# Optimization experiments

Measured on AMD Instinct MI355X. Metric: run time of the kernel, lower is better.

## Reference

```python
import jax, jax.numpy as jnp
import numpy as np

B, C, Q, E = 32, 1024, 64, 256  # batch, max_context_len, max_question_len, embedding_size
FE = 4 * E                      # final_encoding_size (self_attention=False)


def setup_inputs() -> dict:
    key = jax.random.key(0)
    ks = jax.random.split(key, 7)
    return {
        "context": jax.random.normal(ks[0], (B, C, E), dtype=jnp.float32),
        "question": jax.random.normal(ks[1], (B, Q, E), dtype=jnp.float32),
        "context_mask": jnp.ones((B, C), dtype=jnp.float32),
        "w_question": jax.random.normal(ks[2], (E,), dtype=jnp.float32),
        "w_context": jax.random.normal(ks[3], (E,), dtype=jnp.float32),
        "w_multiple": jax.random.normal(ks[4], (E,), dtype=jnp.float32),
        "final_W": jax.random.normal(ks[5], (FE, FE), dtype=jnp.float32) * (1.0 / np.sqrt(FE)),
        "final_b": jnp.zeros((FE,), dtype=jnp.float32),
    }


def reference(context, question, context_mask, w_question, w_context, w_multiple, final_W, final_b):
    # Trilinear similarity: s[b,c,q] = <w_q, q_q> + <w_c, c_c> + <w_m, c_c * q_q>
    q_weighted = question @ w_question                 # (B, Q)
    ctx_weighted = context @ w_context                 # (B, C)
    # (question.unsqueeze(1) * context.unsqueeze(2)) @ w_multiple, computed
    # without materializing the (B, C, Q, E) intermediate:
    mult = jnp.einsum('bce,bqe->bcq', context * w_multiple, question)  # (B, C, Q)
    similarity = ctx_weighted[:, :, None] + q_weighted[:, None, :] + mult  # (B, C, Q)

    # Context-to-query attention (softmax over question dim)
    c2q_att = jnp.einsum('bcq,bqe->bce', jax.nn.softmax(similarity, axis=2), question)

    # Query-to-context attention (softmax over context dim of row-max scores)
    q2c_weights = jax.nn.softmax(jnp.max(similarity, axis=2), axis=1)   # (B, C)
    q2c_att = jnp.einsum('bc,bce->be', q2c_weights, context)            # (B, E)

    attended = jnp.concatenate(
        [context, c2q_att, context * c2q_att, context * q2c_att[:, None, :]],
        axis=2)                                                          # (B, C, 4E)

    # MaskedLinear: affine map, output rows zeroed where context_mask == 0
    out = (attended @ final_W.T + final_b) * context_mask[:, :, None]    # (B, C, 4E)
    return out
```

## Files before the change

kernel.cpp:

```cpp
#include <hip/hip_runtime.h>

#define BB 32
#define CC 1024
#define QQ 64
#define EE 256
#define FE 1024
#define MM (BB*CC)

typedef __bf16 bf16_t;
typedef bf16_t bf16x8 __attribute__((ext_vector_type(8)));
typedef float f32x4 __attribute__((ext_vector_type(4)));

__device__ __forceinline__ unsigned short f2bf(float f) {
  unsigned u = __float_as_uint(f);
  u += 0x7fffu + ((u >> 16) & 1u);
  return (unsigned short)(u >> 16);
}
__device__ __forceinline__ float bf2f(unsigned short u) {
  return __uint_as_float(((unsigned)u) << 16);
}

__device__ __forceinline__ void gload_lds16(const void* g, void* l) {
  __builtin_amdgcn_global_load_lds(
      (const __attribute__((address_space(1))) unsigned int*)g,
      (__attribute__((address_space(3))) unsigned int*)l, 16, 0, 0);
}

__global__ void k_prep_q(const float* __restrict__ question, const float* __restrict__ w_question,
                         const float* __restrict__ w_multiple, float* __restrict__ qm,
                         float* __restrict__ qw) {
  int gid = blockIdx.x * 256 + threadIdx.x;
  int row = gid >> 6;
  int lane = gid & 63;
  const float4 q = *(const float4*)(question + (size_t)row * EE + lane * 4);
  const float4 wm = *(const float4*)(w_multiple + lane * 4);
  const float4 wq = *(const float4*)(w_question + lane * 4);
  float4 r; r.x = q.x*wm.x; r.y = q.y*wm.y; r.z = q.z*wm.z; r.w = q.w*wm.w;
  *(float4*)(qm + (size_t)row * EE + lane * 4) = r;
  float d = q.x*wq.x + q.y*wq.y + q.z*wq.z + q.w*wq.w;
  d += __shfl_xor(d, 1);  d += __shfl_xor(d, 2);  d += __shfl_xor(d, 4);
  d += __shfl_xor(d, 8);  d += __shfl_xor(d, 16); d += __shfl_xor(d, 32);
  if (lane == 0) qw[row] = d;
}

__global__ void k_cast_w(const float* __restrict__ W, unsigned short* __restrict__ Wb) {
  int i = (blockIdx.x * 256 + threadIdx.x) * 4;
  float4 v = *(const float4*)(W + i);
  ushort4 o; o.x = f2bf(v.x); o.y = f2bf(v.y); o.z = f2bf(v.z); o.w = f2bf(v.w);
  *(ushort4*)(Wb + i) = o;
}

#define DOT4(acc, A, Bv) acc += A.x*Bv.x + A.y*Bv.y + A.z*Bv.z + A.w*Bv.w

__launch_bounds__(256)
__global__ void k_sim(const float* __restrict__ ctx, const float* __restrict__ qm,
                      const float* __restrict__ qw_g, const float* __restrict__ w_context,
                      float* __restrict__ P, float* __restrict__ rowmax,
                      unsigned short* __restrict__ att) {
  __shared__ float qml[QQ][260];
  __shared__ float ck[64][36];
  __shared__ float cwl[64];
  __shared__ float qwl[QQ];
  const int tid = threadIdx.x;
  const int b = blockIdx.y;
  const int c0 = blockIdx.x * 64;
  const int tx = tid & 15, ty = tid >> 4;

  const float* qmb = qm + (size_t)b * (QQ * EE);
  for (int idx = tid * 4; idx < QQ * EE; idx += 1024) {
    float4 v = *(const float4*)(qmb + idx);
    *(float4*)&qml[idx >> 8][idx & 255] = v;
  }
  if (tid < QQ) qwl[tid] = qw_g[b * QQ + tid];

  const int cr = tid >> 3, er = (tid & 7) * 4;
  const float* crow0 = ctx + ((size_t)(b * CC + c0 + cr)) * EE;
  const float* crow1 = crow0 + 32 * EE;
  unsigned short* arow0 = att + ((size_t)(b * CC + c0 + cr)) * FE;
  unsigned short* arow1 = arow0 + (size_t)32 * FE;
  float s[4][4] = {{0.f}};
  float cp0 = 0.f, cp1 = 0.f;

  for (int eo = 0; eo < EE; eo += 32) {
    float4 cv0 = *(const float4*)(crow0 + eo + er);
    float4 cv1 = *(const float4*)(crow1 + eo + er);
    float4 wc = *(const float4*)(w_context + eo + er);
    cp0 += cv0.x*wc.x + cv0.y*wc.y + cv0.z*wc.z + cv0.w*wc.w;
    cp1 += cv1.x*wc.x + cv1.y*wc.y + cv1.z*wc.z + cv1.w*wc.w;
    ushort4 u0, u1;
    u0.x = f2bf(cv0.x); u0.y = f2bf(cv0.y); u0.z = f2bf(cv0.z); u0.w = f2bf(cv0.w);
    u1.x = f2bf(cv1.x); u1.y = f2bf(cv1.y); u1.z = f2bf(cv1.z); u1.w = f2bf(cv1.w);
    *(ushort4*)(arow0 + eo + er) = u0;
    *(ushort4*)(arow1 + eo + er) = u1;
    __syncthreads();
    *(float4*)&ck[cr][er] = cv0;
    *(float4*)&ck[cr + 32][er] = cv1;
    __syncthreads();
#pragma unroll
    for (int ee = 0; ee < 32; ee += 4) {
      float4 a0 = *(const float4*)&ck[ty +  0][ee];
      float4 a1 = *(const float4*)&ck[ty + 16][ee];
      float4 a2 = *(const float4*)&ck[ty + 32][ee];
      float4 a3 = *(const float4*)&ck[ty + 48][ee];
      float4 b0 = *(const float4*)&qml[tx +  0][eo + ee];
      float4 b1 = *(const float4*)&qml[tx + 16][eo + ee];
      float4 b2 = *(const float4*)&qml[tx + 32][eo + ee];
      float4 b3 = *(const float4*)&qml[tx + 48][eo + ee];
      DOT4(s[0][0], a0, b0); DOT4(s[0][1], a0, b1); DOT4(s[0][2], a0, b2); DOT4(s[0][3], a0, b3);
      DOT4(s[1][0], a1, b0); DOT4(s[1][1], a1, b1); DOT4(s[1][2], a1, b2); DOT4(s[1][3], a1, b3);
      DOT4(s[2][0], a2, b0); DOT4(s[2][1], a2, b1); DOT4(s[2][2], a2, b2); DOT4(s[2][3], a2, b3);
      DOT4(s[3][0], a3, b0); DOT4(s[3][1], a3, b1); DOT4(s[3][2], a3, b2); DOT4(s[3][3], a3, b3);
    }
  }
  cp0 += __shfl_xor(cp0, 1); cp0 += __shfl_xor(cp0, 2); cp0 += __shfl_xor(cp0, 4);
  cp1 += __shfl_xor(cp1, 1); cp1 += __shfl_xor(cp1, 2); cp1 += __shfl_xor(cp1, 4);
  if ((tid & 7) == 0) { cwl[cr] = cp0; cwl[cr + 32] = cp1; }
  __syncthreads();

#pragma unroll
  for (int i = 0; i < 4; ++i) {
    int c = ty + 16 * i;
    float cw = cwl[c];
    float f[4], mx = -1e30f;
#pragma unroll
    for (int j = 0; j < 4; ++j) {
      f[j] = s[i][j] + cw + qwl[tx + 16 * j];
      mx = fmaxf(mx, f[j]);
    }
    mx = fmaxf(mx, __shfl_xor(mx, 1));
    mx = fmaxf(mx, __shfl_xor(mx, 2));
    mx = fmaxf(mx, __shfl_xor(mx, 4));
    mx = fmaxf(mx, __shfl_xor(mx, 8));
    float sum = 0.f;
#pragma unroll
    for (int j = 0; j < 4; ++j) { f[j] = expf(f[j] - mx); sum += f[j]; }
    sum += __shfl_xor(sum, 1);
    sum += __shfl_xor(sum, 2);
    sum += __shfl_xor(sum, 4);
    sum += __shfl_xor(sum, 8);
    float inv = 1.f / sum;
    if (tx == 0) rowmax[(size_t)b * CC + c0 + c] = mx;
    size_t prow = ((size_t)(b * CC + c0 + c)) * QQ;
#pragma unroll
    for (int j = 0; j < 4; ++j) P[prow + tx + 16 * j] = f[j] * inv;
  }
}

__global__ void k_q2c_softmax(const float* __restrict__ rowmax, float* __restrict__ q2cw) {
  int b = blockIdx.x, tid = threadIdx.x;
  __shared__ float rbuf[4], sbuf[4];
  float4 v = *(const float4*)(rowmax + (size_t)b * CC + tid * 4);
  float m = fmaxf(fmaxf(v.x, v.y), fmaxf(v.z, v.w));
  for (int off = 1; off < 64; off <<= 1) m = fmaxf(m, __shfl_xor(m, off));
  int wv = tid >> 6;
  if ((tid & 63) == 0) rbuf[wv] = m;
  __syncthreads();
  m = fmaxf(fmaxf(rbuf[0], rbuf[1]), fmaxf(rbuf[2], rbuf[3]));
  float e0 = expf(v.x - m), e1 = expf(v.y - m), e2 = expf(v.z - m), e3 = expf(v.w - m);
  float sum = e0 + e1 + e2 + e3;
  for (int off = 1; off < 64; off <<= 1) sum += __shfl_xor(sum, off);
  if ((tid & 63) == 0) sbuf[wv] = sum;
  __syncthreads();
  sum = sbuf[0] + sbuf[1] + sbuf[2] + sbuf[3];
  float inv = 1.f / sum;
  float4 o; o.x = e0 * inv; o.y = e1 * inv; o.z = e2 * inv; o.w = e3 * inv;
  *(float4*)(q2cw + (size_t)b * CC + tid * 4) = o;
}

__global__ void k_q2c_part(const unsigned short* __restrict__ att, const float* __restrict__ w,
                           float* __restrict__ part) {
  int b = blockIdx.y, ch = blockIdx.x;
  int e = threadIdx.x;
  const unsigned short* base = att + ((size_t)(b * CC + ch * 128)) * FE + e;
  const float* wp = w + b * CC + ch * 128;
  float acc = 0.f;
#pragma unroll 4
  for (int c = 0; c < 128; ++c) acc += wp[c] * bf2f(base[(size_t)c * FE]);
  part[(b * 8 + ch) * EE + e] = acc;
}

__global__ void k_q2c_sum(const float* __restrict__ part, float* __restrict__ q2catt) {
  int b = blockIdx.x, e = threadIdx.x;
  float a = 0.f;
#pragma unroll
  for (int ch = 0; ch < 8; ++ch) a += part[(b * 8 + ch) * EE + e];
  q2catt[b * EE + e] = a;
}

__launch_bounds__(256)
__global__ void k_pv(const float* __restrict__ P, const float* __restrict__ question,
                     const float* __restrict__ q2catt, unsigned short* __restrict__ attended) {
  __shared__ float PT[QQ][65];
  __shared__ float ql[QQ][68];
  const int tid = threadIdx.x;
  const int b = blockIdx.y, c0 = blockIdx.x * 64;
  const int tx = tid & 15, ty = tid >> 4;

  {
    int q4 = (tid & 15) * 4, cb = tid >> 4;
#pragma unroll
    for (int r = 0; r < 4; ++r) {
      int c = cb + 16 * r;
      float4 v = *(const float4*)(P + ((size_t)(b * CC + c0 + c)) * QQ + q4);
      PT[q4 + 0][c] = v.x; PT[q4 + 1][c] = v.y; PT[q4 + 2][c] = v.z; PT[q4 + 3][c] = v.w;
    }
  }
  const float* qb = question + (size_t)b * (QQ * EE);
  const float* g2 = q2catt + b * EE;

  for (int ep = 0; ep < EE; ep += 64) {
    __syncthreads();
    {
      int q = tid >> 2, e16 = (tid & 3) * 16;
      const float* src = qb + (size_t)q * EE + ep + e16;
      float4 v0 = *(const float4*)(src);
      float4 v1 = *(const float4*)(src + 4);
      float4 v2 = *(const float4*)(src + 8);
      float4 v3 = *(const float4*)(src + 12);
      *(float4*)&ql[q][e16]      = v0;
      *(float4*)&ql[q][e16 + 4]  = v1;
      *(float4*)&ql[q][e16 + 8]  = v2;
      *(float4*)&ql[q][e16 + 12] = v3;
    }
    __syncthreads();
    float s[4][4] = {{0.f}};
#pragma unroll 8
    for (int q = 0; q < QQ; ++q) {
      float a0 = PT[q][ty];
      float a1 = PT[q][ty + 16];
      float a2 = PT[q][ty + 32];
      float a3 = PT[q][ty + 48];
      float4 bv = *(const float4*)&ql[q][tx * 4];
      s[0][0] += a0 * bv.x; s[0][1] += a0 * bv.y; s[0][2] += a0 * bv.z; s[0][3] += a0 * bv.w;
      s[1][0] += a1 * bv.x; s[1][1] += a1 * bv.y; s[1][2] += a1 * bv.z; s[1][3] += a1 * bv.w;
      s[2][0] += a2 * bv.x; s[2][1] += a2 * bv.y; s[2][2] += a2 * bv.z; s[2][3] += a2 * bv.w;
      s[3][0] += a3 * bv.x; s[3][1] += a3 * bv.y; s[3][2] += a3 * bv.z; s[3][3] += a3 * bv.w;
    }
    float4 gv = *(const float4*)(g2 + ep + tx * 4);
#pragma unroll
    for (int i = 0; i < 4; ++i) {
      int c = ty + 16 * i;
      size_t row = (size_t)(b * CC + c0 + c);
      unsigned short* arow = attended + row * (size_t)FE;
      ushort4 cu = *(const ushort4*)(arow + 0 * EE + ep + tx * 4);
      float cx = bf2f(cu.x), cy = bf2f(cu.y), cz = bf2f(cu.z), cw = bf2f(cu.w);
      ushort4 s1, s2, s3;
      s1.x = f2bf(s[i][0]);        s1.y = f2bf(s[i][1]);        s1.z = f2bf(s[i][2]);        s1.w = f2bf(s[i][3]);
      s2.x = f2bf(cx * s[i][0]);   s2.y = f2bf(cy * s[i][1]);   s2.z = f2bf(cz * s[i][2]);   s2.w = f2bf(cw * s[i][3]);
      s3.x = f2bf(cx * gv.x);      s3.y = f2bf(cy * gv.y);      s3.z = f2bf(cz * gv.z);      s3.w = f2bf(cw * gv.w);
      *(ushort4*)(arow + 1 * EE + ep + tx * 4) = s1;
      *(ushort4*)(arow + 2 * EE + ep + tx * 4) = s2;
      *(ushort4*)(arow + 3 * EE + ep + tx * 4) = s3;
    }
  }
}

__launch_bounds__(512, 2)
__global__ void k_gemm(const unsigned short* __restrict__ A, const unsigned short* __restrict__ Bw,
                       const float* __restrict__ bias, const float* __restrict__ mask,
                       float* __restrict__ out) {
  __shared__ bf16_t As[2][256][64];
  __shared__ bf16_t Bs[2][256][64];
  const int tid = threadIdx.x;
  const int lane = tid & 63;
  const int wave = tid >> 6;
  const int wr = wave >> 2;
  const int wc = wave & 3;

  const int bid = blockIdx.x;
  const int wg = (bid & 7) * 64 + (bid >> 3);
  const int brow = (wg >> 2) * 256;
  const int bcol = (wg & 3) * 256;

  const int r = lane & 15, kg4 = lane >> 4;
  const int lxor = lane & 7;

  const int srow = tid >> 3;
  const int sg = (tid & 7) ^ (srow & 7);
  const unsigned short* gA = A  + (size_t)(brow + srow) * FE + sg * 8;
  const unsigned short* gB = Bw + (size_t)(bcol + srow) * FE + sg * 8;
  bf16_t* ldsA = &As[0][srow][(tid & 7) * 8];
  bf16_t* ldsB = &Bs[0][srow][(tid & 7) * 8];

  f32x4 acc[8][4] = {};

#define STAGE(bufi, t)                                                          \
  {                                                                             \
    const int k0 = (t) * 64;                                                    \
    _Pragma("unroll")                                                           \
    for (int r0 = 0; r0 < 256; r0 += 64) {                                      \
      gload_lds16(gA + (size_t)r0 * FE + k0, ldsA + (size_t)(bufi) * (256*64) + r0 * 64); \
      gload_lds16(gB + (size_t)r0 * FE + k0, ldsB + (size_t)(bufi) * (256*64) + r0 * 64); \
    }                                                                           \
  }

  STAGE(0, 0);
  STAGE(1, 1);

  for (int t = 0; t < 16; ++t) {
    const int cur = t & 1;
    if (t < 15) {
      asm volatile("s_waitcnt vmcnt(8)" ::: "memory");
    } else {
      asm volatile("s_waitcnt vmcnt(0)" ::: "memory");
    }
    __builtin_amdgcn_s_barrier();

    bf16x8 fa[8][2], fb[4][2];
#pragma unroll
    for (int m = 0; m < 8; ++m) {
      const int rowa = wr * 128 + m * 16 + r;
#pragma unroll
      for (int ks = 0; ks < 2; ++ks)
        fa[m][ks] = *(const bf16x8*)&As[cur][rowa][((ks * 4 + kg4) ^ lxor) * 8];
    }
#pragma unroll
    for (int n = 0; n < 4; ++n) {
      const int rowb = wc * 64 + n * 16 + r;
#pragma unroll
      for (int ks = 0; ks < 2; ++ks)
        fb[n][ks] = *(const bf16x8*)&Bs[cur][rowb][((ks * 4 + kg4) ^ lxor) * 8];
    }
    asm volatile("s_waitcnt lgkmcnt(0)" ::: "memory");
    __builtin_amdgcn_s_barrier();

    if (t < 14) STAGE(cur, t + 2);

    __builtin_amdgcn_s_setprio(1);
#pragma unroll
    for (int ks = 0; ks < 2; ++ks)
#pragma unroll
      for (int m = 0; m < 8; ++m)
#pragma unroll
        for (int n = 0; n < 4; ++n)
          acc[m][n] = __builtin_amdgcn_mfma_f32_16x16x32_bf16(fa[m][ks], fb[n][ks], acc[m][n], 0, 0, 0);
    __builtin_amdgcn_s_setprio(0);
  }
#undef STAGE

#pragma unroll
  for (int m = 0; m < 8; ++m) {
#pragma unroll
    for (int n = 0; n < 4; ++n) {
#pragma unroll
      for (int reg = 0; reg < 4; ++reg) {
        int row = brow + wr * 128 + m * 16 + kg4 * 4 + reg;
        int col = bcol + wc * 64 + n * 16 + r;
        out[(size_t)row * FE + col] = (acc[m][n][reg] + bias[col]) * mask[row];
      }
    }
  }
}

extern "C" void kernel_launch(void* const* d_in, const int* in_sizes, int n_in,
                              void* d_out, int out_size, void* d_ws, size_t ws_size,
                              hipStream_t stream) {
  const float* ctx  = (const float*)d_in[0];
  const float* ques = (const float*)d_in[1];
  const float* mask = (const float*)d_in[2];
  const float* w_q  = (const float*)d_in[3];
  const float* w_c  = (const float*)d_in[4];
  const float* w_m  = (const float*)d_in[5];
  const float* fW   = (const float*)d_in[6];
  const float* fb   = (const float*)d_in[7];
  float* out = (float*)d_out;

  char* ws = (char*)d_ws;
  float* qm     = (float*)(ws);
  float* qw     = (float*)(ws + 8388608);
  float* rowmax = (float*)(ws + 8396800);
  float* q2cw   = (float*)(ws + 8527872);
  float* part   = (float*)(ws + 8658944);
  float* q2catt = (float*)(ws + 8921088);
  float* P      = (float*)(ws + 8953856);
  unsigned short* attended = (unsigned short*)(ws + 17342464);
  unsigned short* Wb       = (unsigned short*)(ws + 84451328);

  k_prep_q<<<512, 256, 0, stream>>>(ques, w_q, w_m, qm, qw);
  k_cast_w<<<1024, 256, 0, stream>>>(fW, Wb);
  k_sim<<<dim3(16, 32), 256, 0, stream>>>(ctx, qm, qw, w_c, P, rowmax, attended);
  k_q2c_softmax<<<32, 256, 0, stream>>>(rowmax, q2cw);
  k_q2c_part<<<dim3(8, 32), 256, 0, stream>>>(attended, q2cw, part);
  k_q2c_sum<<<32, 256, 0, stream>>>(part, q2catt);
  k_pv<<<dim3(16, 32), 256, 0, stream>>>(P, ques, q2catt, attended);
  k_gemm<<<512, 512, 0, stream>>>(attended, Wb, fb, mask, out);
}
```

Baseline: 178.5 us.

## Restructure GEMM main loop into 8-wave ping-pong with split half-tile staging

Rewrites the bf16 GEMM main loop so each K-tile's A and B are staged as two 128-row halves. LDS fragment reads, global-to-LDS loads and four MFMA sub-blocks are interleaved per iteration under frequent barriers and partial vmcnt waits. The aim is to overlap global loads and LDS reads with MFMA work at finer grain than whole-tile double buffering. It adds many barriers and a tightly choreographed wait scheme that may serialize waves or carry subtle race risks.

```diff
diff --git a/kernel.cpp b/kernel.cpp
--- a/kernel.cpp
+++ b/kernel.cpp
@@ -259,13 +259,14 @@
 __global__ void k_gemm(const unsigned short* __restrict__ A, const unsigned short* __restrict__ Bw,
                        const float* __restrict__ bias, const float* __restrict__ mask,
                        float* __restrict__ out) {
-  __shared__ bf16_t As[2][256][64];
-  __shared__ bf16_t Bs[2][256][64];
+  __shared__ bf16_t As[2][2][128][64];
+  __shared__ bf16_t Bs[2][2][128][64];
   const int tid = threadIdx.x;
   const int lane = tid & 63;
   const int wave = tid >> 6;
   const int wr = wave >> 2;
   const int wc = wave & 3;
+  const int bh = wc >> 1;
 
   const int bid = blockIdx.x;
   const int wg = (bid & 7) * 64 + (bid >> 3);
@@ -273,70 +274,100 @@
   const int bcol = (wg & 3) * 256;
 
   const int r = lane & 15, kg4 = lane >> 4;
-  const int lxor = lane & 7;
+  const int rx = r & 7;
 
   const int srow = tid >> 3;
   const int sg = (tid & 7) ^ (srow & 7);
-  const unsigned short* gA = A  + (size_t)(brow + srow) * FE + sg * 8;
-  const unsigned short* gB = Bw + (size_t)(bcol + srow) * FE + sg * 8;
-  bf16_t* ldsA = &As[0][srow][(tid & 7) * 8];
-  bf16_t* ldsB = &Bs[0][srow][(tid & 7) * 8];
+  const unsigned short* gAb = A  + (size_t)(brow + srow) * FE + sg * 8;
+  const unsigned short* gBb = Bw + (size_t)(bcol + srow) * FE + sg * 8;
+  bf16_t* ldsAb = &As[0][0][srow][(tid & 7) * 8];
+  bf16_t* ldsBb = &Bs[0][0][srow][(tid & 7) * 8];
 
   f32x4 acc[8][4] = {};
-
-#define STAGE(bufi, t)                                                          \
-  {                                                                             \
-    const int k0 = (t) * 64;                                                    \
-    _Pragma("unroll")                                                           \
-    for (int r0 = 0; r0 < 256; r0 += 64) {                                      \
-      gload_lds16(gA + (size_t)r0 * FE + k0, ldsA + (size_t)(bufi) * (256*64) + r0 * 64); \
-      gload_lds16(gB + (size_t)r0 * FE + k0, ldsB + (size_t)(bufi) * (256*64) + r0 * 64); \
-    }                                                                           \
-  }
-
-  STAGE(0, 0);
-  STAGE(1, 1);
-
-  for (int t = 0; t < 16; ++t) {
-    const int cur = t & 1;
-    if (t < 15) {
-      asm volatile("s_waitcnt vmcnt(8)" ::: "memory");
-    } else {
-      asm volatile("s_waitcnt vmcnt(0)" ::: "memory");
-    }
-    __builtin_amdgcn_s_barrier();
-
-    bf16x8 fa[8][2], fb[4][2];
-#pragma unroll
-    for (int m = 0; m < 8; ++m) {
-      const int rowa = wr * 128 + m * 16 + r;
-#pragma unroll
-      for (int ks = 0; ks < 2; ++ks)
-        fa[m][ks] = *(const bf16x8*)&As[cur][rowa][((ks * 4 + kg4) ^ lxor) * 8];
-    }
-#pragma unroll
-    for (int n = 0; n < 4; ++n) {
-      const int rowb = wc * 64 + n * 16 + r;
-#pragma unroll
-      for (int ks = 0; ks < 2; ++ks)
-        fb[n][ks] = *(const bf16x8*)&Bs[cur][rowb][((ks * 4 + kg4) ^ lxor) * 8];
-    }
-    asm volatile("s_waitcnt lgkmcnt(0)" ::: "memory");
-    __builtin_amdgcn_s_barrier();
-
-    if (t < 14) STAGE(cur, t + 2);
-
-    __builtin_amdgcn_s_setprio(1);
-#pragma unroll
-    for (int ks = 0; ks < 2; ++ks)
-#pragma unroll
-      for (int m = 0; m < 8; ++m)
-#pragma unroll
-        for (int n = 0; n < 4; ++n)
-          acc[m][n] = __builtin_amdgcn_mfma_f32_16x16x32_bf16(fa[m][ks], fb[n][ks], acc[m][n], 0, 0, 0);
-    __builtin_amdgcn_s_setprio(0);
-  }
-#undef STAGE
+  bf16x8 faA[4][2], faB[4][2], fbA[2][2], fbB[2][2];
+
+#define BARX __builtin_amdgcn_s_barrier()
+#define LGKM0 do { asm volatile("s_waitcnt lgkmcnt(0)" ::: "memory"); __builtin_amdgcn_sched_barrier(0); } while (0)
+#define VMW4 asm volatile("s_waitcnt vmcnt(4)" ::: "memory")
+#define VMW0 asm volatile("s_waitcnt vmcnt(0)" ::: "memory")
+
+#define ST_A(SLOT, H, KOFF) do {                                              \
+    const unsigned short* s_ = gAb + (size_t)((H) * 128) * FE + (KOFF);       \
+    bf16_t* d_ = ldsAb + ((SLOT) * 2 + (H)) * (128 * 64);                     \
+    gload_lds16(s_, d_);                                                      \
+    gload_lds16(s_ + (size_t)64 * FE, d_ + 64 * 64);                          \
+  } while (0)
+#define ST_B(SLOT, H, KOFF) do {                                              \
+    const unsigned short* s_ = gBb + (size_t)((H) * 128) * FE + (KOFF);       \
+    bf16_t* d_ = ldsBb + ((SLOT) * 2 + (H)) * (128 * 64);                     \
+    gload_lds16(s_, d_);                                                      \
+    gload_lds16(s_ + (size_t)64 * FE, d_ + 64 * 64);                          \
+  } while (0)
+
+#define RD_FA(DST, SLOT, MB) do {                                             \
+    _Pragma("unroll") for (int mm = 0; mm < 4; ++mm) {                        \
+      const int row_ = ((MB) + mm) * 16 + r;                                  \
+      _Pragma("unroll") for (int ks = 0; ks < 2; ++ks)                        \
+        DST[mm][ks] = *(const bf16x8*)&As[SLOT][wr][row_][((ks * 4 + kg4) ^ rx) * 8]; \
+    } } while (0)
+#define RD_FB(DST, SLOT, NB) do {                                             \
+    _Pragma("unroll") for (int nn = 0; nn < 2; ++nn) {                        \
+      const int row_ = (wc & 1) * 64 + ((NB) + nn) * 16 + r;                  \
+      _Pragma("unroll") for (int ks = 0; ks < 2; ++ks)                        \
+        DST[nn][ks] = *(const bf16x8*)&Bs[SLOT][bh][row_][((ks * 4 + kg4) ^ rx) * 8]; \
+    } } while (0)
+
+#define MFMA16(FA, FB, MB, NB) do {                                           \
+    __builtin_amdgcn_s_setprio(1);                                            \
+    _Pragma("unroll") for (int ks = 0; ks < 2; ++ks)                          \
+    _Pragma("unroll") for (int mm = 0; mm < 4; ++mm)                          \
+    _Pragma("unroll") for (int nn = 0; nn < 2; ++nn)                          \
+      acc[(MB) + mm][(NB) + nn] = __builtin_amdgcn_mfma_f32_16x16x32_bf16(    \
+          FA[mm][ks], FB[nn][ks], acc[(MB) + mm][(NB) + nn], 0, 0, 0);        \
+    __builtin_amdgcn_s_setprio(0);                                            \
+  } while (0)
+
+  ST_B(0, 0, 0);  ST_B(0, 1, 0);  ST_A(0, 0, 0);  ST_A(0, 1, 0);
+  ST_B(1, 0, 64); ST_B(1, 1, 64);
+  VMW4;
+  BARX;
+
+#pragma unroll 1
+  for (int i = 0; i < 8; ++i) {
+    const int kT1 = (2 * i + 1) * 64;
+    const int kT2 = (2 * i + 2) * 64;
+    const int kT3 = (2 * i + 3) * 64;
+    const bool more = (i < 7);
+
+    RD_FA(faA, 0, 0); RD_FB(fbA, 0, 0);
+    ST_A(1, 0, kT1);
+    BARX; LGKM0; MFMA16(faA, fbA, 0, 0); BARX;
+    RD_FB(fbB, 0, 2);
+    ST_A(1, 1, kT1);
+    BARX; LGKM0; MFMA16(faA, fbB, 0, 2); BARX;
+    RD_FA(faB, 0, 4);
+    if (more) ST_B(0, 0, kT2);
+    BARX; LGKM0; MFMA16(faB, fbA, 4, 0); BARX;
+    if (more) { ST_B(0, 1, kT2); VMW4; } else { VMW0; }
+    BARX; MFMA16(faB, fbB, 4, 2); BARX;
+
+    RD_FA(faA, 1, 0); RD_FB(fbA, 1, 0);
+    if (more) ST_A(0, 0, kT2);
+    BARX; LGKM0; MFMA16(faA, fbA, 0, 0); BARX;
+    RD_FB(fbB, 1, 2);
+    if (more) ST_A(0, 1, kT2);
+    BARX; LGKM0; MFMA16(faA, fbB, 0, 2); BARX;
+    RD_FA(faB, 1, 4);
+    if (more) ST_B(1, 0, kT3);
+    BARX; LGKM0; MFMA16(faB, fbA, 4, 0); BARX;
+    if (more) { ST_B(1, 1, kT3); VMW4; }
+    BARX; MFMA16(faB, fbB, 4, 2); BARX;
+  }
+#undef ST_A
+#undef ST_B
+#undef RD_FA
+#undef RD_FB
+#undef MFMA16
 
 #pragma unroll
   for (int m = 0; m < 8; ++m) {
```

Result: slower. 184.2 us (+3.2%).
